# Kernel tuning notes

Hardware: AMD Instinct MI355X
Metric: run time of the kernel (lower is better)

The kernel has to match this reference:

```python
import jax, jax.numpy as jnp
import numpy as np

N = 50000; E = 320000; DIN = 768; D = 256; R = 4; L = 3
B = 64; T = 6; SD = 128; SH = 256; NC = 14; ALPHA = 0.15
NEG = -1e30


def setup_inputs():
    keys = iter(jax.random.split(jax.random.key(0), 64))
    def nrm(shape, s=0.02):
        return s * jax.random.normal(next(keys), shape, dtype=jnp.float32)
    inp = {}
    inp["x"] = jax.random.normal(next(keys), (N, DIN), dtype=jnp.float32)
    inp["edge_index"] = jax.random.randint(next(keys), (2, E), 0, N)
    inp["edge_type"] = jax.random.randint(next(keys), (E,), 0, R)
    inp["batch"] = jnp.sort(jax.random.randint(next(keys), (N,), 0, B))
    inp["sequence"] = jax.random.normal(next(keys), (B, T, SD), dtype=jnp.float32)
    inp["proj_W"] = nrm((D, DIN)); inp["proj_b"] = nrm((D,))
    inp["Wr"] = nrm((L, R, D, D))
    inp["Ws"] = nrm((L, D, D)); inp["bs"] = nrm((L, D))
    inp["att_W1"] = nrm((L, R, D // 2, 2 * D)); inp["att_b1"] = nrm((L, R, D // 2))
    inp["att_W2"] = nrm((L, R, D // 2)); inp["att_b2"] = nrm((L, R))
    inp["emb"] = nrm((L, R, D // 4), 0.1)
    inp["imp"] = jnp.tile(jnp.array([1.2, 1.1, 1.4, 0.9], dtype=jnp.float32), (L, 1))
    inp["ln_g"] = jnp.ones((L, D), jnp.float32); inp["ln_b"] = jnp.zeros((L, D), jnp.float32)
    inp["gm_W1"] = nrm((D // 2, D)); inp["gm_b1"] = nrm((D // 2,))
    inp["gm_W2"] = nrm((D // 4, D // 2)); inp["gm_b2"] = nrm((D // 4,))
    inp["gm_W3"] = nrm((NC, D // 4)); inp["gm_b3"] = nrm((NC,))
    inp["gru_Wih"] = nrm((2, 3 * SH, SD)); inp["gru_Whh"] = nrm((2, 3 * SH, SH))
    inp["gru_bih"] = nrm((2, 3 * SH)); inp["gru_bhh"] = nrm((2, 3 * SH))
    inp["sm_W1"] = nrm((SH, 2 * SH)); inp["sm_b1"] = nrm((SH,))
    inp["sm_W2"] = nrm((SH // 2, SH)); inp["sm_b2"] = nrm((SH // 2,))
    inp["sm_W3"] = nrm((NC, SH // 2)); inp["sm_b3"] = nrm((NC,))
    return inp


def _gru_dir(x, Wih, Whh, bih, bhh):  # x: [B,T,SD] -> [B,T,SH], torch GRU equations
    def step(h, xt):
        gi = xt @ Wih.T + bih
        gh = h @ Whh.T + bhh
        ir, iz, in_ = jnp.split(gi, 3, axis=-1)
        hr, hz, hn = jnp.split(gh, 3, axis=-1)
        r = jax.nn.sigmoid(ir + hr)
        z = jax.nn.sigmoid(iz + hz)
        n = jnp.tanh(in_ + r * hn)
        h = (1.0 - z) * n + z * h
        return h, h
    h0 = jnp.zeros((x.shape[0], Whh.shape[1]), x.dtype)
    _, ys = jax.lax.scan(step, h0, jnp.swapaxes(x, 0, 1))
    return jnp.swapaxes(ys, 0, 1)


def _gnn_layer(h, h0, src, dst, et, Wr, Ws, bs, aW1, ab1, aW2, ab2, emb, imp, g, b):
    ew = jax.nn.softmax(imp)  # layer_edge_importance softmax over R types
    cat = jnp.concatenate([h[dst], h[src]], axis=1)  # [E, 2D] = [x_i, x_j]
    agg = jnp.zeros_like(h)
    for r in range(R):
        tx = h @ Wr[r].T  # [N, D] per-type transform
        s = jax.nn.relu(cat @ aW1[r].T + ab1[r]) @ aW2[r] + ab2[r]  # [E]
        s = jax.nn.leaky_relu(s, 0.2) + jnp.mean(emb[r])
        mask = et == r
        a = jax.nn.softmax(jnp.where(mask, s, NEG))  # softmax over all type-r edges (dim=0 in torch)
        a = jnp.where(mask, a, 0.0)
        msg = jax.ops.segment_sum(a[:, None] * tx[src], dst, num_segments=h.shape[0])
        agg = agg + ew[r] * msg
    out = (1.0 - ALPHA) * agg + h @ Ws.T + bs + ALPHA * h0
    mu = jnp.mean(out, axis=-1, keepdims=True)
    var = jnp.var(out, axis=-1, keepdims=True)
    out = (out - mu) / jnp.sqrt(var + 1e-5) * g + b  # LayerNorm (eps=1e-5)
    return jax.nn.gelu(out, approximate=False)


def _forward(x, sequence, proj_W, proj_b, Wr, Ws, bs, att_W1, att_b1, att_W2, att_b2, emb, imp, ln_g, ln_b, gm_W1, gm_b1, gm_W2, gm_b2, gm_W3, gm_b3, gru_Wih, gru_Whh, gru_bih, gru_bhh, sm_W1, sm_b1, sm_W2, sm_b2, sm_W3, sm_b3, edge_index, edge_type, batch):
    # sequence branch: bidirectional GRU, avg+max pool over time, MLP readout
    fwd = _gru_dir(sequence, gru_Wih[0], gru_Whh[0], gru_bih[0], gru_bhh[0])
    bwd = _gru_dir(sequence[:, ::-1], gru_Wih[1], gru_Whh[1], gru_bih[1], gru_bhh[1])[:, ::-1]
    seq_out = jnp.concatenate([fwd, bwd], axis=-1)  # [B, T, 2*SH]
    z = jnp.mean(seq_out, axis=1) + jnp.max(seq_out, axis=1)
    z = jax.nn.relu(z @ sm_W1.T + sm_b1)
    z = jax.nn.relu(z @ sm_W2.T + sm_b2)
    seq_logits = z @ sm_W3.T + sm_b3
    # graph branch
    src, dst = edge_index[0], edge_index[1]
    h = x @ proj_W.T + proj_b
    h0 = h
    for i in range(L):
        h = _gnn_layer(h, h0, src, dst, edge_type, Wr[i], Ws[i], bs[i], att_W1[i], att_b1[i], att_W2[i], att_b2[i], emb[i], imp[i], ln_g[i], ln_b[i])
    sums = jax.ops.segment_sum(h, batch, num_segments=B)
    cnt = jax.ops.segment_sum(jnp.ones((h.shape[0],), h.dtype), batch, num_segments=B)
    pooled = sums / jnp.clip(cnt, 1.0)[:, None]  # global_mean_pool
    gz = jax.nn.relu(pooled @ gm_W1.T + gm_b1)
    gz = jax.nn.relu(gz @ gm_W2.T + gm_b2)
    graph_logits = gz @ gm_W3.T + gm_b3
    return graph_logits + seq_logits


def reference(x, edge_index, edge_type, batch, sequence, proj_W, proj_b, Wr, Ws, bs, att_W1, att_b1, att_W2, att_b2, emb, imp, ln_g, ln_b, gm_W1, gm_b1, gm_W2, gm_b2, gm_W3, gm_b3, gru_Wih, gru_Whh, gru_bih, gru_bhh, sm_W1, sm_b1, sm_W2, sm_b2, sm_W3, sm_b3):
    return _forward(x, sequence, proj_W, proj_b, Wr, Ws, bs, att_W1, att_b1, att_W2, att_b2, emb, imp, ln_g, ln_b, gm_W1, gm_b1, gm_W2, gm_b2, gm_W3, gm_b3, gru_Wih, gru_Whh, gru_bih, gru_bhh, sm_W1, sm_b1, sm_W2, sm_b2, sm_W3, sm_b3, edge_index, edge_type, batch)
```

## Files before the change

kernel.cpp:

```cpp
#include <hip/hip_runtime.h>
#include <math.h>

#define N_NODES 50000
#define E_EDGES 320000
#define DIN_    768
#define D_      256
#define R_TYPES 4
#define L_LAYERS 3
#define BATCH_  64
#define T_STEPS 6
#define SD_     128
#define SH_     256
#define NC_     14
#define ALPHA_  0.15f
#define NBLK_B  1250
#define POOL_CHUNK 256
#define E_PAD   (E_EDGES + 256)
#define SCAN_BLK 49
#define NCAT    (D_ + R_TYPES * D_)

typedef __bf16 bf16_t;
typedef bf16_t bf16x8_t __attribute__((ext_vector_type(8)));
typedef bf16_t bf16x4_t __attribute__((ext_vector_type(4)));
typedef float  f32x4_t  __attribute__((ext_vector_type(4)));

__device__ __forceinline__ f32x4_t mfma16(bf16x8_t a, bf16x8_t b, f32x4_t c) {
    return __builtin_amdgcn_mfma_f32_16x16x32_bf16(a, b, c, 0, 0, 0);
}

__global__ void f2b_kernel(const float* __restrict__ src, bf16_t* __restrict__ dst, int n4)
{
    for (int i = blockIdx.x * blockDim.x + threadIdx.x; i < n4; i += gridDim.x * blockDim.x) {
        float4 v = ((const float4*)src)[i];
        bf16_t o[4] = {(bf16_t)v.x, (bf16_t)v.y, (bf16_t)v.z, (bf16_t)v.w};
        *(ulong1*)&dst[i * 4] = *(ulong1*)o;
    }
}

__global__ void pack_wcat_kernel(const float* __restrict__ Ws, const float* __restrict__ Wr,
                                 bf16_t* __restrict__ Wcat)
{
    int total = L_LAYERS * NCAT * D_;
    for (int i = blockIdx.x * blockDim.x + threadIdx.x; i < total; i += gridDim.x * blockDim.x) {
        int l = i / (NCAT * D_);
        int rem = i - l * NCAT * D_;
        int row = rem / D_, k = rem - row * D_;
        float v = (row < D_) ? Ws[((size_t)l * D_ + row) * D_ + k]
                             : Wr[((size_t)l * R_TYPES * D_ + (row - D_)) * D_ + k];
        Wcat[i] = (bf16_t)v;
    }
}

__global__ void transpose2_kernel(const float* __restrict__ in, float* __restrict__ out, int R, int C)
{
    int total = 2 * R * C;
    for (int i = blockIdx.x * blockDim.x + threadIdx.x; i < total; i += gridDim.x * blockDim.x) {
        int dir = i / (R * C);
        int rem = i - dir * R * C;
        int r = rem / C, c = rem - r * C;
        out[dir * R * C + c * R + r] = in[i];
    }
}

__global__ __launch_bounds__(256) void proj_mfma(
    const float* __restrict__ A, const bf16_t* __restrict__ W,
    const float* __restrict__ bias, float* __restrict__ outf,
    bf16_t* __restrict__ outb, int M)
{
    __shared__ bf16_t As[64][44];
    __shared__ bf16_t Bs[256][44];
    const int m0 = blockIdx.x * 64;
    const int tid = threadIdx.x;
    const int wave = tid >> 6, lane = tid & 63;
    const int q = lane >> 4, c = lane & 15;
    const int srow = tid >> 2, skq = tid & 3;

    f32x4_t acc[4][4] = {};
    for (int k0 = 0; k0 < DIN_; k0 += 32) {
        {
            int m = m0 + srow;
            bf16_t tmp[8] = {};
            if (m < M) {
                float4 v0 = *(const float4*)&A[(size_t)m * DIN_ + k0 + skq * 8];
                float4 v1 = *(const float4*)&A[(size_t)m * DIN_ + k0 + skq * 8 + 4];
                tmp[0] = (bf16_t)v0.x; tmp[1] = (bf16_t)v0.y; tmp[2] = (bf16_t)v0.z; tmp[3] = (bf16_t)v0.w;
                tmp[4] = (bf16_t)v1.x; tmp[5] = (bf16_t)v1.y; tmp[6] = (bf16_t)v1.z; tmp[7] = (bf16_t)v1.w;
            }
            *(bf16x8_t*)&As[srow][skq * 8] = *(bf16x8_t*)tmp;
            #pragma unroll
            for (int i = 0; i < 4; i++) {
                int nrow = srow + 64 * i;
                *(bf16x8_t*)&Bs[nrow][skq * 8] = *(const bf16x8_t*)&W[(size_t)nrow * DIN_ + k0 + skq * 8];
            }
        }
        __syncthreads();
        bf16x8_t af[4], bfv[4];
        #pragma unroll
        for (int mt = 0; mt < 4; mt++) af[mt] = *(const bf16x8_t*)&As[mt * 16 + c][q * 8];
        #pragma unroll
        for (int nt = 0; nt < 4; nt++) bfv[nt] = *(const bf16x8_t*)&Bs[wave * 64 + nt * 16 + c][q * 8];
        #pragma unroll
        for (int mt = 0; mt < 4; mt++)
            #pragma unroll
            for (int nt = 0; nt < 4; nt++)
                acc[mt][nt] = mfma16(af[mt], bfv[nt], acc[mt][nt]);
        __syncthreads();
    }
    #pragma unroll
    for (int nt = 0; nt < 4; nt++) {
        int n = wave * 64 + nt * 16 + c;
        float bv = bias[n];
        #pragma unroll
        for (int mt = 0; mt < 4; mt++) {
            #pragma unroll
            for (int j = 0; j < 4; j++) {
                int m = m0 + mt * 16 + q * 4 + j;
                if (m < M) {
                    float v = acc[mt][nt][j] + bv;
                    outf[(size_t)m * D_ + n] = v;
                    outb[(size_t)m * D_ + n] = (bf16_t)v;
                }
            }
        }
    }
}

__global__ __launch_bounds__(256) void linear_dual_mfma(
    const bf16_t* __restrict__ A, const bf16_t* __restrict__ W,
    const float* __restrict__ bias, float* __restrict__ outf,
    bf16_t* __restrict__ outb, int M)
{
    __shared__ bf16_t As[64][44];
    __shared__ bf16_t Bs[64][44];
    const int m0 = blockIdx.x * 64;
    const int n0 = blockIdx.y * 64;
    const int tid = threadIdx.x;
    const int wave = tid >> 6, lane = tid & 63;
    const int wy = wave >> 1, wx = wave & 1;
    const int q = lane >> 4, c = lane & 15;
    const int srow = tid >> 2, skq = tid & 3;

    f32x4_t acc[2][2] = {};
    for (int k0 = 0; k0 < D_; k0 += 32) {
        {
            int m = m0 + srow;
            bf16x8_t av = {};
            if (m < M) av = *(const bf16x8_t*)&A[(size_t)m * D_ + k0 + skq * 8];
            *(bf16x8_t*)&As[srow][skq * 8] = av;
            *(bf16x8_t*)&Bs[srow][skq * 8] = *(const bf16x8_t*)&W[(size_t)(n0 + srow) * D_ + k0 + skq * 8];
        }
        __syncthreads();
        bf16x8_t af[2], bfv[2];
        #pragma unroll
        for (int mt = 0; mt < 2; mt++) af[mt] = *(const bf16x8_t*)&As[wy * 32 + mt * 16 + c][q * 8];
        #pragma unroll
        for (int nt = 0; nt < 2; nt++) bfv[nt] = *(const bf16x8_t*)&Bs[wx * 32 + nt * 16 + c][q * 8];
        #pragma unroll
        for (int mt = 0; mt < 2; mt++)
            #pragma unroll
            for (int nt = 0; nt < 2; nt++)
                acc[mt][nt] = mfma16(af[mt], bfv[nt], acc[mt][nt]);
        __syncthreads();
    }
    #pragma unroll
    for (int mt = 0; mt < 2; mt++) {
        #pragma unroll
        for (int nt = 0; nt < 2; nt++) {
            int n = n0 + wx * 32 + nt * 16 + c;
            float bv = (n < D_) ? bias[n] : 0.0f;
            #pragma unroll
            for (int j = 0; j < 4; j++) {
                int m = m0 + wy * 32 + mt * 16 + q * 4 + j;
                if (m < M) {
                    float v = acc[mt][nt][j] + bv;
                    if (n < D_) outf[(size_t)m * D_ + n] = v;
                    else        outb[(size_t)m * (R_TYPES * D_) + (n - D_)] = (bf16_t)v;
                }
            }
        }
    }
}

__global__ __launch_bounds__(256) void bucket_count2(const int* __restrict__ et,
                                                     int* __restrict__ blockCnt)
{
    int b = blockIdx.x, tid = threadIdx.x;
    int r = et[b * 256 + tid];
    int lane = tid & 63, wv = tid >> 6;
    __shared__ int wcnt[4][4];
    #pragma unroll
    for (int t = 0; t < 4; t++) {
        unsigned long long m = __ballot(r == t);
        if (lane == 0) wcnt[wv][t] = __popcll(m);
    }
    __syncthreads();
    if (tid < 4)
        blockCnt[b * 4 + tid] = wcnt[0][tid] + wcnt[1][tid] + wcnt[2][tid] + wcnt[3][tid];
}

__global__ void bucket_scan(const int* __restrict__ blockCnt, int* __restrict__ boffP,
                            int* __restrict__ cnt, int* __restrict__ basePerBlock,
                            int* __restrict__ bsrc, int* __restrict__ bdst)
{
    __shared__ int tot[4];
    int t = threadIdx.x;
    if (t < 4) {
        int s = 0;
        for (int b = 0; b < NBLK_B; b++) s += blockCnt[b * 4 + t];
        tot[t] = s;
    }
    __syncthreads();
    if (t == 0) {
        int o = 0;
        for (int r = 0; r < 4; r++) {
            boffP[r] = o; cnt[r] = tot[r];
            o += (tot[r] + 63) & ~63;
        }
        boffP[4] = o;
    }
    __syncthreads();
    if (t < 4) {
        int run = boffP[t];
        for (int b = 0; b < NBLK_B; b++) { basePerBlock[b * 4 + t] = run; run += blockCnt[b * 4 + t]; }
    }
    __syncthreads();
    for (int r = 0; r < 4; r++) {
        int s = boffP[r] + cnt[r], e = boffP[r + 1];
        for (int i = s + t; i < e; i += 64) { bsrc[i] = 0; bdst[i] = 0; }
    }
}

__global__ __launch_bounds__(256) void bucket_scatter2(
    const int* __restrict__ ei, const int* __restrict__ et,
    const int* __restrict__ basePerBlock, int* __restrict__ bsrc, int* __restrict__ bdst)
{
    int b = blockIdx.x, tid = threadIdx.x;
    int e = b * 256 + tid;
    int r = et[e];
    int lane = tid & 63, wv = tid >> 6;
    __shared__ int wcnt[4][4];
    int myrank = 0;
    unsigned long long ltmask = (1ull << lane) - 1ull;
    #pragma unroll
    for (int t = 0; t < 4; t++) {
        unsigned long long m = __ballot(r == t);
        if (r == t) myrank = __popcll(m & ltmask);
        if (lane == 0) wcnt[wv][t] = __popcll(m);
    }
    __syncthreads();
    int wbase = 0;
    for (int w = 0; w < wv; w++) wbase += wcnt[w][r];
    int pos = basePerBlock[b * 4 + r] + wbase + myrank;
    bsrc[pos] = ei[e];
    bdst[pos] = ei[E_EDGES + e];
}

__global__ void embmean_kernel(const float* __restrict__ emb, float* __restrict__ em)
{
    int lr = threadIdx.x;
    if (lr < L_LAYERS * R_TYPES) {
        float s = 0.0f;
        for (int k = 0; k < 64; k++) s += emb[lr * 64 + k];
        em[lr] = s / 64.0f;
    }
}

__global__ __launch_bounds__(256) void deg_count_kernel(
    const int* __restrict__ bdst, const int* __restrict__ boffP, const int* __restrict__ cnt,
    int* __restrict__ deg)
{
    __shared__ int sb[5], sc[4];
    if (threadIdx.x < 5) sb[threadIdx.x] = boffP[threadIdx.x];
    if (threadIdx.x < 4) sc[threadIdx.x] = cnt[threadIdx.x];
    __syncthreads();
    int total = sb[4];
    for (int p = blockIdx.x * blockDim.x + threadIdx.x; p < total; p += gridDim.x * blockDim.x) {
        int r = 0; while (r < 3 && p >= sb[r + 1]) r++;
        if (p - sb[r] < sc[r]) atomicAdd(&deg[bdst[p]], 1);
    }
}

__global__ __launch_bounds__(256) void scan1_kernel(const int* __restrict__ deg,
                                                    int* __restrict__ rowptr, int* __restrict__ blockSum)
{
    __shared__ int sdata[256];
    int b = blockIdx.x, t = threadIdx.x;
    int idx0 = b * 1024 + t * 4;
    int d[4];
    #pragma unroll
    for (int j = 0; j < 4; j++) d[j] = (idx0 + j < N_NODES) ? deg[idx0 + j] : 0;
    int tsum = d[0] + d[1] + d[2] + d[3];
    sdata[t] = tsum;
    __syncthreads();
    for (int off = 1; off < 256; off <<= 1) {
        int v = (t >= off) ? sdata[t - off] : 0;
        __syncthreads();
        sdata[t] += v;
        __syncthreads();
    }
    int ex = sdata[t] - tsum;
    int acc = ex;
    #pragma unroll
    for (int j = 0; j < 4; j++) {
        if (idx0 + j < N_NODES) rowptr[idx0 + j] = acc;
        acc += d[j];
    }
    if (t == 255) blockSum[b] = sdata[255];
}

__global__ void scan2_kernel(const int* __restrict__ blockSum, int* __restrict__ blockOff)
{
    if (threadIdx.x == 0) {
        int o = 0;
        for (int b = 0; b < SCAN_BLK; b++) { blockOff[b] = o; o += blockSum[b]; }
    }
}

__global__ __launch_bounds__(256) void scan3_kernel(int* __restrict__ rowptr,
                                                    const int* __restrict__ blockOff,
                                                    int* __restrict__ cursor)
{
    int idx = blockIdx.x * blockDim.x + threadIdx.x;
    if (idx < N_NODES) {
        int v = rowptr[idx] + blockOff[idx >> 10];
        rowptr[idx] = v; cursor[idx] = v;
    }
    if (idx == 0) rowptr[N_NODES] = E_EDGES;
}

__global__ __launch_bounds__(256) void csr_scatter_kernel(
    const int* __restrict__ bsrc, const int* __restrict__ bdst,
    const int* __restrict__ boffP, const int* __restrict__ cnt,
    int* __restrict__ cursor, int* __restrict__ csrSrc, int* __restrict__ csrPos)
{
    __shared__ int sb[5], sc[4];
    if (threadIdx.x < 5) sb[threadIdx.x] = boffP[threadIdx.x];
    if (threadIdx.x < 4) sc[threadIdx.x] = cnt[threadIdx.x];
    __syncthreads();
    int total = sb[4];
    for (int p = blockIdx.x * blockDim.x + threadIdx.x; p < total; p += gridDim.x * blockDim.x) {
        int r = 0; while (r < 3 && p >= sb[r + 1]) r++;
        if (p - sb[r] < sc[r]) {
            int pos = atomicAdd(&cursor[bdst[p]], 1);
            csrSrc[pos] = bsrc[p];
            csrPos[pos] = p;
        }
    }
}

__global__ __launch_bounds__(256) void attn_mfma(
    const bf16_t* __restrict__ hb, const int* __restrict__ bsrc, const int* __restrict__ bdst,
    const int* __restrict__ boffP, const int* __restrict__ cnt, int l,
    const bf16_t* __restrict__ W1base, const float* __restrict__ b1base,
    const float* __restrict__ W2base, const float* __restrict__ b2base,
    const float* __restrict__ em, float* __restrict__ sbuf)
{
    const int p0 = blockIdx.x * 64;
    if (p0 >= boffP[4]) return;
    int r = 0;
    while (r < 3 && p0 >= boffP[r + 1]) r++;
    const int lr = l * R_TYPES + r;
    const int base = boffP[r];
    const int cnt_r = cnt[r];
    const bf16_t* W1 = W1base + (size_t)lr * 128 * 512;
    const float*  b1 = b1base + lr * 128;
    const float*  W2 = W2base + lr * 128;

    __shared__ int nd_d[64], nd_s[64];
    __shared__ bf16_t Acat[64][44];
    __shared__ bf16_t Bs[128][44];
    const int tid = threadIdx.x;
    if (tid < 64) nd_d[tid] = bdst[p0 + tid];
    else if (tid < 128) nd_s[tid - 64] = bsrc[p0 + tid - 64];
    __syncthreads();
    const int wave = tid >> 6, lane = tid & 63;
    const int q = lane >> 4, c = lane & 15;
    const int srow = tid >> 2, skq = tid & 3;

    f32x4_t acc[8] = {};
    for (int ks = 0; ks < 16; ks++) {
        {
            int node = (ks < 8) ? nd_d[srow] : nd_s[srow];
            int koffm = (ks & 7) * 32 + skq * 8;
            *(bf16x8_t*)&Acat[srow][skq * 8] = *(const bf16x8_t*)&hb[(size_t)node * D_ + koffm];
            #pragma unroll
            for (int s = 0; s < 2; s++) {
                int slot = tid + s * 256;
                int nrow = slot >> 2, nkq = slot & 3;
                *(bf16x8_t*)&Bs[nrow][nkq * 8] = *(const bf16x8_t*)&W1[(size_t)nrow * 512 + ks * 32 + nkq * 8];
            }
        }
        __syncthreads();
        bf16x8_t af = *(const bf16x8_t*)&Acat[wave * 16 + c][q * 8];
        #pragma unroll
        for (int nt = 0; nt < 8; nt++) {
            bf16x8_t bfv = *(const bf16x8_t*)&Bs[nt * 16 + c][q * 8];
            acc[nt] = mfma16(af, bfv, acc[nt]);
        }
        __syncthreads();
    }
    float part[4] = {0, 0, 0, 0};
    #pragma unroll
    for (int nt = 0; nt < 8; nt++) {
        int n = nt * 16 + c;
        float b1v = b1[n], w2v = W2[n];
        #pragma unroll
        for (int j = 0; j < 4; j++) {
            float v = acc[nt][j] + b1v;
            v = v > 0.0f ? v : 0.0f;
            part[j] += v * w2v;
        }
    }
    #pragma unroll
    for (int j = 0; j < 4; j++) {
        #pragma unroll
        for (int mask = 1; mask <= 8; mask <<= 1)
            part[j] += __shfl_xor(part[j], mask);
    }
    if (c == 0) {
        float b2v = b2base[lr], emv = em[lr];
        #pragma unroll
        for (int j = 0; j < 4; j++) {
            int p = p0 + wave * 16 + q * 4 + j;
            bool valid = (p - base) < cnt_r;
            float sv = part[j] + b2v;
            sv = sv > 0.0f ? sv : 0.2f * sv;
            sbuf[p] = valid ? (sv + emv) : -1e30f;
        }
    }
}

__device__ __forceinline__ unsigned fkey(float f) {
    unsigned u = __float_as_uint(f);
    return (u & 0x80000000u) ? ~u : (u | 0x80000000u);
}
__device__ __forceinline__ float fkey_inv(unsigned k) {
    unsigned u = (k & 0x80000000u) ? (k ^ 0x80000000u) : ~k;
    return __uint_as_float(u);
}

__global__ void bucket_max_kernel(const float* __restrict__ sbuf, const int* __restrict__ boffP,
                                  unsigned* __restrict__ redl)
{
    int r = blockIdx.y;
    int lo = boffP[r], hi = boffP[r + 1];
    float m = -1e30f;
    for (int i = lo + blockIdx.x * blockDim.x + threadIdx.x; i < hi; i += gridDim.x * blockDim.x)
        m = fmaxf(m, sbuf[i]);
    for (int o = 32; o; o >>= 1) m = fmaxf(m, __shfl_down(m, o));
    __shared__ float wm[4];
    int lane = threadIdx.x & 63, wv = threadIdx.x >> 6;
    if (lane == 0) wm[wv] = m;
    __syncthreads();
    if (threadIdx.x == 0) {
        float b = fmaxf(fmaxf(wm[0], wm[1]), fmaxf(wm[2], wm[3]));
        atomicMax(&redl[r * 2], fkey(b));
    }
}

__global__ void bucket_sum_kernel(const float* __restrict__ sbuf, const int* __restrict__ boffP,
                                  unsigned* __restrict__ redl)
{
    int r = blockIdx.y;
    int lo = boffP[r], hi = boffP[r + 1];
    float mxf = fkey_inv(redl[r * 2]);
    float s = 0.0f;
    for (int i = lo + blockIdx.x * blockDim.x + threadIdx.x; i < hi; i += gridDim.x * blockDim.x)
        s += expf(sbuf[i] - mxf);
    for (int o = 32; o; o >>= 1) s += __shfl_down(s, o);
    __shared__ float wm[4];
    int lane = threadIdx.x & 63, wv = threadIdx.x >> 6;
    if (lane == 0) wm[wv] = s;
    __syncthreads();
    if (threadIdx.x == 0) atomicAdd((float*)&redl[r * 2 + 1], wm[0] + wm[1] + wm[2] + wm[3]);
}

__global__ __launch_bounds__(256) void msg_ln_gelu_kernel(
    const float* __restrict__ sbuf, const bf16_t* __restrict__ txAll,
    const int* __restrict__ csrSrc, const int* __restrict__ csrPos,
    const int* __restrict__ rowptr, const int* __restrict__ boffP,
    const unsigned* __restrict__ redl, const float* __restrict__ imp, int l,
    const float* __restrict__ accb, const float* __restrict__ h0,
    const float* __restrict__ g, const float* __restrict__ bvec,
    float* __restrict__ h, bf16_t* __restrict__ hb)
{
    __shared__ float smx[4], sinv[4], scoef[4];
    __shared__ int sb[5];
    if (threadIdx.x == 0) {
        float e0 = expf(imp[l * 4 + 0]), e1 = expf(imp[l * 4 + 1]);
        float e2 = expf(imp[l * 4 + 2]), e3 = expf(imp[l * 4 + 3]);
        float den = e0 + e1 + e2 + e3;
        float ews[4] = {e0 / den, e1 / den, e2 / den, e3 / den};
        for (int r = 0; r < 4; r++) {
            smx[r] = fkey_inv(redl[r * 2]);
            sinv[r] = 1.0f / ((const float*)redl)[r * 2 + 1];
            scoef[r] = (1.0f - ALPHA_) * ews[r];
        }
        for (int r = 0; r <= 4; r++) sb[r] = boffP[r];
    }
    __syncthreads();
    int n = blockIdx.x * 4 + (threadIdx.x >> 6);
    if (n >= N_NODES) return;
    int lane = threadIdx.x & 63;
    int c4 = lane * 4;
    float msg[4] = {0, 0, 0, 0};
    int i0 = rowptr[n], i1 = rowptr[n + 1];
    for (int i = i0; i < i1; i++) {
        int src = csrSrc[i];
        int p = csrPos[i];
        int r = 0; while (r < 3 && p >= sb[r + 1]) r++;
        float a = expf(sbuf[p] - smx[r]) * sinv[r] * scoef[r];
        bf16x4_t tv = *(const bf16x4_t*)&txAll[(size_t)src * (R_TYPES * D_) + r * D_ + c4];
        msg[0] += a * (float)tv[0];
        msg[1] += a * (float)tv[1];
        msg[2] += a * (float)tv[2];
        msg[3] += a * (float)tv[3];
    }
    float4 ac = *(const float4*)&accb[(size_t)n * D_ + c4];
    float4 hz = *(const float4*)&h0[(size_t)n * D_ + c4];
    float v[4];
    v[0] = msg[0] + ac.x + ALPHA_ * hz.x;
    v[1] = msg[1] + ac.y + ALPHA_ * hz.y;
    v[2] = msg[2] + ac.z + ALPHA_ * hz.z;
    v[3] = msg[3] + ac.w + ALPHA_ * hz.w;
    float sum = v[0] + v[1] + v[2] + v[3];
    #pragma unroll
    for (int o = 32; o; o >>= 1) sum += __shfl_down(sum, o);
    sum = __shfl(sum, 0);
    float mean = sum * (1.0f / 256.0f);
    float sq = 0.0f;
    #pragma unroll
    for (int j = 0; j < 4; j++) { float d = v[j] - mean; sq += d * d; }
    #pragma unroll
    for (int o = 32; o; o >>= 1) sq += __shfl_down(sq, o);
    sq = __shfl(sq, 0);
    float rstd = rsqrtf(sq * (1.0f / 256.0f) + 1e-5f);
    float4 gg = *(const float4*)&g[c4];
    float4 bb = *(const float4*)&bvec[c4];
    float ga[4] = {gg.x, gg.y, gg.z, gg.w};
    float ba[4] = {bb.x, bb.y, bb.z, bb.w};
    float outv[4];
    bf16_t outb[4];
    #pragma unroll
    for (int j = 0; j < 4; j++) {
        float x = (v[j] - mean) * rstd * ga[j] + ba[j];
        float ge = 0.5f * x * (1.0f + erff(x * 0.7071067811865475f));
        outv[j] = ge;
        outb[j] = (bf16_t)ge;
    }
    *(float4*)&h[(size_t)n * D_ + c4] = *(float4*)outv;
    *(bf16x4_t*)&hb[(size_t)n * D_ + c4] = *(bf16x4_t*)outb;
}

__global__ __launch_bounds__(256) void pool_seg_kernel(
    const float* __restrict__ h, const int* __restrict__ batch,
    float* __restrict__ pooled, float* __restrict__ cntb, int Nn)
{
    int start = blockIdx.x * POOL_CHUNK;
    if (start >= Nn) return;
    int end = start + POOL_CHUNK; if (end > Nn) end = Nn;
    int c = threadIdx.x;
    __shared__ int bseg[POOL_CHUNK];
    if (start + c < Nn) bseg[c] = batch[start + c];
    __syncthreads();
    float acc = 0.0f;
    int cur = bseg[0];
    int segcnt = 0;
    for (int node = start; node < end; node++) {
        int b = bseg[node - start];
        if (b != cur) {
            atomicAdd(&pooled[cur * D_ + c], acc);
            if (c == 0) atomicAdd(&cntb[cur], (float)segcnt);
            acc = 0.0f; segcnt = 0; cur = b;
        }
        acc += h[(size_t)node * D_ + c];
        segcnt++;
    }
    atomicAdd(&pooled[cur * D_ + c], acc);
    if (c == 0) atomicAdd(&cntb[cur], (float)segcnt);
}

__global__ __launch_bounds__(256) void final_mlp_kernel(
    const float* __restrict__ pooled, const float* __restrict__ cntb,
    const float* __restrict__ W1, const float* __restrict__ b1,
    const float* __restrict__ W2, const float* __restrict__ b2,
    const float* __restrict__ W3, const float* __restrict__ b3,
    const float* __restrict__ seqlg, float* __restrict__ out)
{
    int b = blockIdx.x;
    int t = threadIdx.x;
    __shared__ float p[256];
    __shared__ float z1[128];
    __shared__ float z2[64];
    float c = cntb[b]; c = c < 1.0f ? 1.0f : c;
    p[t] = pooled[b * 256 + t] / c;
    __syncthreads();
    if (t < 128) {
        float s = b1[t];
        for (int k = 0; k < 256; k++) s += p[k] * W1[t * 256 + k];
        z1[t] = s > 0.0f ? s : 0.0f;
    }
    __syncthreads();
    if (t < 64) {
        float s = b2[t];
        for (int k = 0; k < 128; k++) s += z1[k] * W2[t * 128 + k];
        z2[t] = s > 0.0f ? s : 0.0f;
    }
    __syncthreads();
    if (t < NC_) {
        float s = b3[t];
        for (int k = 0; k < 64; k++) s += z2[k] * W3[t * 64 + k];
        out[b * NC_ + t] = s + seqlg[b * NC_ + t];
    }
}

__global__ __launch_bounds__(768) void gru_gi_kernel(
    const float* __restrict__ seq, const float* __restrict__ WihT,
    const float* __restrict__ bih, float* __restrict__ gi)
{
    int blk = blockIdx.x;
    int dir = blk >> 6, b = blk & 63;
    __shared__ float xt[T_STEPS * SD_];
    int j = threadIdx.x;
    xt[j] = seq[(size_t)b * T_STEPS * SD_ + j];
    __syncthreads();
    const float* Wt = WihT + (size_t)dir * SD_ * 768;
    float av[T_STEPS] = {};
    for (int k = 0; k < SD_; k++) {
        float w = Wt[(size_t)k * 768 + j];
        #pragma unroll
        for (int t = 0; t < T_STEPS; t++) av[t] += xt[t * SD_ + k] * w;
    }
    float bv = bih[dir * 768 + j];
    for (int t = 0; t < T_STEPS; t++)
        gi[(((size_t)blk) * T_STEPS + t) * 768 + j] = av[t] + bv;
}

__global__ __launch_bounds__(768) void gru_step2(
    const float* __restrict__ gi, const float* __restrict__ WhhT,
    const float* __restrict__ bhh, float* __restrict__ hstate,
    float* __restrict__ outs, int t)
{
    int blk = blockIdx.x;
    int dir = blk >> 6;
    int tin = dir ? (T_STEPS - 1 - t) : t;
    __shared__ float hs[SH_];
    __shared__ float gh[768];
    int j = threadIdx.x;
    if (j < SH_) hs[j] = hstate[(size_t)blk * SH_ + j];
    __syncthreads();
    const float* Wt = WhhT + (size_t)dir * SH_ * 768;
    float a = bhh[dir * 768 + j];
    for (int k = 0; k < SH_; k++)
        a += hs[k] * Wt[(size_t)k * 768 + j];
    gh[j] = a;
    __syncthreads();
    if (j < SH_) {
        size_t gib = (((size_t)blk) * T_STEPS + tin) * 768;
        float r = 1.0f / (1.0f + expf(-(gi[gib + j] + gh[j])));
        float z = 1.0f / (1.0f + expf(-(gi[gib + 256 + j] + gh[256 + j])));
        float n = tanhf(gi[gib + 512 + j] + r * gh[512 + j]);
        float hn = (1.0f - z) * n + z * hs[j];
        hstate[(size_t)blk * SH_ + j] = hn;
        outs[(((size_t)blk) * T_STEPS + tin) * SH_ + j] = hn;
    }
}

__global__ __launch_bounds__(256) void seq_mlp_kernel(
    const float* __restrict__ outs, const float* __restrict__ W1, const float* __restrict__ b1,
    const float* __restrict__ W2, const float* __restrict__ b2,
    const float* __restrict__ W3, const float* __restrict__ b3,
    float* __restrict__ seqlg)
{
    int b = blockIdx.x;
    int t = threadIdx.x;
    __shared__ float z[512];
    __shared__ float z1[256];
    __shared__ float z2[128];
    for (int c = t; c < 512; c += 256) {
        int dir = c >> 8, cc = c & 255;
        float mean = 0.0f, mx = -1e30f;
        for (int tt = 0; tt < T_STEPS; tt++) {
            float v = outs[(((size_t)dir * 64 + b) * T_STEPS + tt) * SH_ + cc];
            mean += v; mx = fmaxf(mx, v);
        }
        z[c] = mean * (1.0f / T_STEPS) + mx;
    }
    __syncthreads();
    {
        float s = b1[t];
        for (int k = 0; k < 512; k++) s += z[k] * W1[t * 512 + k];
        z1[t] = s > 0.0f ? s : 0.0f;
    }
    __syncthreads();
    if (t < 128) {
        float s = b2[t];
        for (int k = 0; k < 256; k++) s += z1[k] * W2[t * 256 + k];
        z2[t] = s > 0.0f ? s : 0.0f;
    }
    __syncthreads();
    if (t < NC_) {
        float s = b3[t];
        for (int k = 0; k < 128; k++) s += z2[k] * W3[t * 128 + k];
        seqlg[b * NC_ + t] = s;
    }
}

extern "C" void kernel_launch(void* const* d_in, const int* in_sizes, int n_in,
                              void* d_out, int out_size, void* d_ws, size_t ws_size,
                              hipStream_t stream)
{
    const float* x      = (const float*)d_in[0];
    const int*   ei     = (const int*)d_in[1];
    const int*   et     = (const int*)d_in[2];
    const int*   batch  = (const int*)d_in[3];
    const float* seq    = (const float*)d_in[4];
    const float* proj_W = (const float*)d_in[5];
    const float* proj_b = (const float*)d_in[6];
    const float* Wr     = (const float*)d_in[7];
    const float* Ws     = (const float*)d_in[8];
    const float* bs     = (const float*)d_in[9];
    const float* aW1    = (const float*)d_in[10];
    const float* ab1    = (const float*)d_in[11];
    const float* aW2    = (const float*)d_in[12];
    const float* ab2    = (const float*)d_in[13];
    const float* emb    = (const float*)d_in[14];
    const float* imp    = (const float*)d_in[15];
    const float* ln_g   = (const float*)d_in[16];
    const float* ln_b   = (const float*)d_in[17];
    const float* gmW1   = (const float*)d_in[18];
    const float* gmb1   = (const float*)d_in[19];
    const float* gmW2   = (const float*)d_in[20];
    const float* gmb2   = (const float*)d_in[21];
    const float* gmW3   = (const float*)d_in[22];
    const float* gmb3   = (const float*)d_in[23];
    const float* gWih   = (const float*)d_in[24];
    const float* gWhh   = (const float*)d_in[25];
    const float* gbih   = (const float*)d_in[26];
    const float* gbhh   = (const float*)d_in[27];
    const float* smW1   = (const float*)d_in[28];
    const float* smb1   = (const float*)d_in[29];
    const float* smW2   = (const float*)d_in[30];
    const float* smb2   = (const float*)d_in[31];
    const float* smW3   = (const float*)d_in[32];
    const float* smb3   = (const float*)d_in[33];
    float* out = (float*)d_out;

    char* ws = (char*)d_ws;
    size_t o = 0;
    auto alloc = [&](size_t bytes) -> void* {
        void* p = ws + o;
        o += (bytes + 1023) & ~(size_t)1023;
        return p;
    };
    float*  h0     = (float*)alloc(sizeof(float) * (size_t)N_NODES * D_);
    float*  h      = (float*)alloc(sizeof(float) * (size_t)N_NODES * D_);
    float*  accb   = (float*)alloc(sizeof(float) * (size_t)N_NODES * D_);
    bf16_t* hbb    = (bf16_t*)alloc(sizeof(bf16_t) * (size_t)N_NODES * D_);
    bf16_t* txAll  = (bf16_t*)alloc(sizeof(bf16_t) * (size_t)N_NODES * R_TYPES * D_);
    bf16_t* projWb = (bf16_t*)alloc(sizeof(bf16_t) * D_ * DIN_);
    bf16_t* Wcat   = (bf16_t*)alloc(sizeof(bf16_t) * L_LAYERS * NCAT * D_);
    bf16_t* aW1b   = (bf16_t*)alloc(sizeof(bf16_t) * L_LAYERS * R_TYPES * 128 * 512);
    float*  sbuf   = (float*)alloc(sizeof(float) * E_PAD);
    int*    bsrc   = (int*)alloc(sizeof(int) * E_PAD);
    int*    bdst   = (int*)alloc(sizeof(int) * E_PAD);
    int*    boffP  = (int*)alloc(sizeof(int) * 8);
    int*    cnt    = (int*)alloc(sizeof(int) * 8);
    int*    blockCnt = (int*)alloc(sizeof(int) * NBLK_B * 4);
    int*    basePerBlock = (int*)alloc(sizeof(int) * NBLK_B * 4);
    int*    deg    = (int*)alloc(sizeof(int) * N_NODES);
    int*    rowptr = (int*)alloc(sizeof(int) * (N_NODES + 8));
    int*    cursor = (int*)alloc(sizeof(int) * N_NODES);
    int*    blockSum = (int*)alloc(sizeof(int) * 64);
    int*    blockOff = (int*)alloc(sizeof(int) * 64);
    int*    csrSrc = (int*)alloc(sizeof(int) * E_EDGES);
    int*    csrPos = (int*)alloc(sizeof(int) * E_EDGES);
    unsigned* red  = (unsigned*)alloc(sizeof(unsigned) * 32);
    float*  em     = (float*)alloc(sizeof(float) * 16);
    float*  seqlg  = (float*)alloc(sizeof(float) * BATCH_ * NC_);
    float*  WihT   = (float*)alloc(sizeof(float) * 2 * SD_ * 768);
    float*  WhhT   = (float*)alloc(sizeof(float) * 2 * SH_ * 768);
    float*  gi     = (float*)alloc(sizeof(float) * 2 * BATCH_ * T_STEPS * 768);
    float*  gruH   = (float*)alloc(sizeof(float) * 2 * BATCH_ * SH_);
    float*  gruO   = (float*)alloc(sizeof(float) * 2 * BATCH_ * T_STEPS * SH_);
    float*  pooled = (float*)alloc(sizeof(float) * BATCH_ * D_);
    float*  cntb   = (float*)alloc(sizeof(float) * BATCH_);
    (void)ws_size; (void)in_sizes; (void)n_in; (void)out_size;

    hipMemsetAsync(red, 0, 32 * sizeof(unsigned), stream);
    hipMemsetAsync(gruH, 0, 2 * BATCH_ * SH_ * sizeof(float), stream);
    hipMemsetAsync(pooled, 0, BATCH_ * D_ * sizeof(float), stream);
    hipMemsetAsync(cntb, 0, BATCH_ * sizeof(float), stream);
    hipMemsetAsync(deg, 0, N_NODES * sizeof(int), stream);

    f2b_kernel<<<64, 256, 0, stream>>>(proj_W, projWb, D_ * DIN_ / 4);
    pack_wcat_kernel<<<512, 256, 0, stream>>>(Ws, Wr, Wcat);
    f2b_kernel<<<256, 256, 0, stream>>>(aW1, aW1b, L_LAYERS * R_TYPES * 128 * 512 / 4);
    transpose2_kernel<<<96, 256, 0, stream>>>(gWih, WihT, 768, SD_);
    transpose2_kernel<<<192, 256, 0, stream>>>(gWhh, WhhT, 768, SH_);

    bucket_count2<<<NBLK_B, 256, 0, stream>>>(et, blockCnt);
    bucket_scan<<<1, 64, 0, stream>>>(blockCnt, boffP, cnt, basePerBlock, bsrc, bdst);
    bucket_scatter2<<<NBLK_B, 256, 0, stream>>>(ei, et, basePerBlock, bsrc, bdst);
    embmean_kernel<<<1, 64, 0, stream>>>(emb, em);

    deg_count_kernel<<<1024, 256, 0, stream>>>(bdst, boffP, cnt, deg);
    scan1_kernel<<<SCAN_BLK, 256, 0, stream>>>(deg, rowptr, blockSum);
    scan2_kernel<<<1, 64, 0, stream>>>(blockSum, blockOff);
    scan3_kernel<<<(N_NODES + 255) / 256, 256, 0, stream>>>(rowptr, blockOff, cursor);
    csr_scatter_kernel<<<1024, 256, 0, stream>>>(bsrc, bdst, boffP, cnt, cursor, csrSrc, csrPos);

    gru_gi_kernel<<<128, 768, 0, stream>>>(seq, WihT, gbih, gi);
    for (int t = 0; t < T_STEPS; t++)
        gru_step2<<<128, 768, 0, stream>>>(gi, WhhT, gbhh, gruH, gruO, t);
    seq_mlp_kernel<<<BATCH_, 256, 0, stream>>>(gruO, smW1, smb1, smW2, smb2, smW3, smb3, seqlg);

    const int MB = (N_NODES + 63) / 64;
    proj_mfma<<<MB, 256, 0, stream>>>(x, projWb, proj_b, h0, hbb, N_NODES);
    const int ATTN_BLKS = E_PAD / 64;
    for (int l = 0; l < L_LAYERS; l++) {
        linear_dual_mfma<<<dim3(MB, NCAT / 64), 256, 0, stream>>>(
            hbb, Wcat + (size_t)l * NCAT * D_, bs + l * D_, accb, txAll, N_NODES);
        attn_mfma<<<ATTN_BLKS, 256, 0, stream>>>(hbb, bsrc, bdst, boffP, cnt, l,
                                                 aW1b, ab1, aW2, ab2, em, sbuf);
        bucket_max_kernel<<<dim3(256, 4), 256, 0, stream>>>(sbuf, boffP, red + l * 8);
        bucket_sum_kernel<<<dim3(256, 4), 256, 0, stream>>>(sbuf, boffP, red + l * 8);
        msg_ln_gelu_kernel<<<(N_NODES + 3) / 4, 256, 0, stream>>>(
            sbuf, txAll, csrSrc, csrPos, rowptr, boffP, red + l * 8, imp, l,
            accb, h0, ln_g + l * D_, ln_b + l * D_, h, hbb);
    }

    pool_seg_kernel<<<(N_NODES + POOL_CHUNK - 1) / POOL_CHUNK, 256, 0, stream>>>(h, batch, pooled, cntb, N_NODES);
    final_mlp_kernel<<<BATCH_, 256, 0, stream>>>(pooled, cntb, gmW1, gmb1, gmW2, gmb2, gmW3, gmb3, seqlg, out);
}
```

Baseline: 1.663 ms.

## Fuse GRU steps, pre-convert x to bf16, drop fp32 layer output

Merges the GRU input projection and all time steps into a single kernel that keeps the hidden state in shared memory, removing per-step launches. The input x is converted to bf16 once and the projection GEMM is split into a 2D grid of 64x64 tiles. The fp32 copy of the layer output is no longer written, and mean pooling reads the bf16 copy instead. This adds an extra conversion pass over x and slightly lowers pooling precision.

```diff
diff --git a/kernel.cpp b/kernel.cpp
--- a/kernel.cpp
+++ b/kernel.cpp
@@ -62,59 +62,52 @@
     }
 }
 
-__global__ __launch_bounds__(256) void proj_mfma(
-    const float* __restrict__ A, const bf16_t* __restrict__ W,
+__global__ __launch_bounds__(256) void proj_mfma3(
+    const bf16_t* __restrict__ A, const bf16_t* __restrict__ W,
     const float* __restrict__ bias, float* __restrict__ outf,
     bf16_t* __restrict__ outb, int M)
 {
     __shared__ bf16_t As[64][44];
-    __shared__ bf16_t Bs[256][44];
+    __shared__ bf16_t Bs[64][44];
     const int m0 = blockIdx.x * 64;
+    const int n0 = blockIdx.y * 64;
     const int tid = threadIdx.x;
     const int wave = tid >> 6, lane = tid & 63;
+    const int wy = wave >> 1, wx = wave & 1;
     const int q = lane >> 4, c = lane & 15;
     const int srow = tid >> 2, skq = tid & 3;
 
-    f32x4_t acc[4][4] = {};
+    f32x4_t acc[2][2] = {};
     for (int k0 = 0; k0 < DIN_; k0 += 32) {
         {
             int m = m0 + srow;
-            bf16_t tmp[8] = {};
-            if (m < M) {
-                float4 v0 = *(const float4*)&A[(size_t)m * DIN_ + k0 + skq * 8];
-                float4 v1 = *(const float4*)&A[(size_t)m * DIN_ + k0 + skq * 8 + 4];
-                tmp[0] = (bf16_t)v0.x; tmp[1] = (bf16_t)v0.y; tmp[2] = (bf16_t)v0.z; tmp[3] = (bf16_t)v0.w;
-                tmp[4] = (bf16_t)v1.x; tmp[5] = (bf16_t)v1.y; tmp[6] = (bf16_t)v1.z; tmp[7] = (bf16_t)v1.w;
-            }
-            *(bf16x8_t*)&As[srow][skq * 8] = *(bf16x8_t*)tmp;
+            bf16x8_t av = {};
+            if (m < M) av = *(const bf16x8_t*)&A[(size_t)m * DIN_ + k0 + skq * 8];
+            *(bf16x8_t*)&As[srow][skq * 8] = av;
+            *(bf16x8_t*)&Bs[srow][skq * 8] = *(const bf16x8_t*)&W[(size_t)(n0 + srow) * DIN_ + k0 + skq * 8];
+        }
+        __syncthreads();
+        bf16x8_t af[2], bfv[2];
+        #pragma unroll
+        for (int mt = 0; mt < 2; mt++) af[mt] = *(const bf16x8_t*)&As[wy * 32 + mt * 16 + c][q * 8];
+        #pragma unroll
+        for (int nt = 0; nt < 2; nt++) bfv[nt] = *(const bf16x8_t*)&Bs[wx * 32 + nt * 16 + c][q * 8];
+        #pragma unroll
+        for (int mt = 0; mt < 2; mt++)
             #pragma unroll
-            for (int i = 0; i < 4; i++) {
-                int nrow = srow + 64 * i;
-                *(bf16x8_t*)&Bs[nrow][skq * 8] = *(const bf16x8_t*)&W[(size_t)nrow * DIN_ + k0 + skq * 8];
-            }
-        }
-        __syncthreads();
-        bf16x8_t af[4], bfv[4];
-        #pragma unroll
-        for (int mt = 0; mt < 4; mt++) af[mt] = *(const bf16x8_t*)&As[mt * 16 + c][q * 8];
-        #pragma unroll
-        for (int nt = 0; nt < 4; nt++) bfv[nt] = *(const bf16x8_t*)&Bs[wave * 64 + nt * 16 + c][q * 8];
-        #pragma unroll
-        for (int mt = 0; mt < 4; mt++)
-            #pragma unroll
-            for (int nt = 0; nt < 4; nt++)
+            for (int nt = 0; nt < 2; nt++)
                 acc[mt][nt] = mfma16(af[mt], bfv[nt], acc[mt][nt]);
         __syncthreads();
     }
     #pragma unroll
-    for (int nt = 0; nt < 4; nt++) {
-        int n = wave * 64 + nt * 16 + c;
-        float bv = bias[n];
-        #pragma unroll
-        for (int mt = 0; mt < 4; mt++) {
+    for (int mt = 0; mt < 2; mt++) {
+        #pragma unroll
+        for (int nt = 0; nt < 2; nt++) {
+            int n = n0 + wx * 32 + nt * 16 + c;
+            float bv = bias[n];
             #pragma unroll
             for (int j = 0; j < 4; j++) {
-                int m = m0 + mt * 16 + q * 4 + j;
+                int m = m0 + wy * 32 + mt * 16 + q * 4 + j;
                 if (m < M) {
                     float v = acc[mt][nt][j] + bv;
                     outf[(size_t)m * D_ + n] = v;
@@ -482,7 +475,7 @@
     const unsigned* __restrict__ redl, const float* __restrict__ imp, int l,
     const float* __restrict__ accb, const float* __restrict__ h0,
     const float* __restrict__ g, const float* __restrict__ bvec,
-    float* __restrict__ h, bf16_t* __restrict__ hb)
+    bf16_t* __restrict__ hb)
 {
     __shared__ float smx[4], sinv[4], scoef[4];
     __shared__ int sb[5];
@@ -539,21 +532,18 @@
     float4 bb = *(const float4*)&bvec[c4];
     float ga[4] = {gg.x, gg.y, gg.z, gg.w};
     float ba[4] = {bb.x, bb.y, bb.z, bb.w};
-    float outv[4];
     bf16_t outb[4];
     #pragma unroll
     for (int j = 0; j < 4; j++) {
         float x = (v[j] - mean) * rstd * ga[j] + ba[j];
         float ge = 0.5f * x * (1.0f + erff(x * 0.7071067811865475f));
-        outv[j] = ge;
         outb[j] = (bf16_t)ge;
     }
-    *(float4*)&h[(size_t)n * D_ + c4] = *(float4*)outv;
     *(bf16x4_t*)&hb[(size_t)n * D_ + c4] = *(bf16x4_t*)outb;
 }
 
 __global__ __launch_bounds__(256) void pool_seg_kernel(
-    const float* __restrict__ h, const int* __restrict__ batch,
+    const bf16_t* __restrict__ hb, const int* __restrict__ batch,
     float* __restrict__ pooled, float* __restrict__ cntb, int Nn)
 {
     int start = blockIdx.x * POOL_CHUNK;
@@ -573,7 +563,7 @@
             if (c == 0) atomicAdd(&cntb[cur], (float)segcnt);
             acc = 0.0f; segcnt = 0; cur = b;
         }
-        acc += h[(size_t)node * D_ + c];
+        acc += (float)hb[(size_t)node * D_ + c];
         segcnt++;
     }
     atomicAdd(&pooled[cur * D_ + c], acc);
@@ -614,55 +604,48 @@
     }
 }
 
-__global__ __launch_bounds__(768) void gru_gi_kernel(
+__global__ __launch_bounds__(768) void gru_full(
     const float* __restrict__ seq, const float* __restrict__ WihT,
-    const float* __restrict__ bih, float* __restrict__ gi)
+    const float* __restrict__ bih, const float* __restrict__ WhhT,
+    const float* __restrict__ bhh, float* __restrict__ outs)
 {
     int blk = blockIdx.x;
     int dir = blk >> 6, b = blk & 63;
     __shared__ float xt[T_STEPS * SD_];
+    __shared__ float hs[SH_];
+    __shared__ float gh[768];
+    __shared__ float gg[768];
     int j = threadIdx.x;
     xt[j] = seq[(size_t)b * T_STEPS * SD_ + j];
-    __syncthreads();
-    const float* Wt = WihT + (size_t)dir * SD_ * 768;
+    if (j < SH_) hs[j] = 0.0f;
+    __syncthreads();
+    const float* Wti = WihT + (size_t)dir * SD_ * 768;
     float av[T_STEPS] = {};
     for (int k = 0; k < SD_; k++) {
-        float w = Wt[(size_t)k * 768 + j];
+        float w = Wti[(size_t)k * 768 + j];
         #pragma unroll
         for (int t = 0; t < T_STEPS; t++) av[t] += xt[t * SD_ + k] * w;
     }
-    float bv = bih[dir * 768 + j];
-    for (int t = 0; t < T_STEPS; t++)
-        gi[(((size_t)blk) * T_STEPS + t) * 768 + j] = av[t] + bv;
-}
-
-__global__ __launch_bounds__(768) void gru_step2(
-    const float* __restrict__ gi, const float* __restrict__ WhhT,
-    const float* __restrict__ bhh, float* __restrict__ hstate,
-    float* __restrict__ outs, int t)
-{
-    int blk = blockIdx.x;
-    int dir = blk >> 6;
-    int tin = dir ? (T_STEPS - 1 - t) : t;
-    __shared__ float hs[SH_];
-    __shared__ float gh[768];
-    int j = threadIdx.x;
-    if (j < SH_) hs[j] = hstate[(size_t)blk * SH_ + j];
-    __syncthreads();
-    const float* Wt = WhhT + (size_t)dir * SH_ * 768;
-    float a = bhh[dir * 768 + j];
-    for (int k = 0; k < SH_; k++)
-        a += hs[k] * Wt[(size_t)k * 768 + j];
-    gh[j] = a;
-    __syncthreads();
-    if (j < SH_) {
-        size_t gib = (((size_t)blk) * T_STEPS + tin) * 768;
-        float r = 1.0f / (1.0f + expf(-(gi[gib + j] + gh[j])));
-        float z = 1.0f / (1.0f + expf(-(gi[gib + 256 + j] + gh[256 + j])));
-        float n = tanhf(gi[gib + 512 + j] + r * gh[512 + j]);
-        float hn = (1.0f - z) * n + z * hs[j];
-        hstate[(size_t)blk * SH_ + j] = hn;
-        outs[(((size_t)blk) * T_STEPS + tin) * SH_ + j] = hn;
+    float bihv = bih[dir * 768 + j];
+    float bhhv = bhh[dir * 768 + j];
+    const float* Wth = WhhT + (size_t)dir * SH_ * 768;
+    for (int t = 0; t < T_STEPS; t++) {
+        int tin = dir ? (T_STEPS - 1 - t) : t;
+        float a = bhhv;
+        for (int k = 0; k < SH_; k++)
+            a += hs[k] * Wth[(size_t)k * 768 + j];
+        gh[j] = a;
+        gg[j] = av[tin] + bihv;
+        __syncthreads();
+        if (j < SH_) {
+            float r = 1.0f / (1.0f + expf(-(gg[j] + gh[j])));
+            float z = 1.0f / (1.0f + expf(-(gg[256 + j] + gh[256 + j])));
+            float n = tanhf(gg[512 + j] + r * gh[512 + j]);
+            float hn = (1.0f - z) * n + z * hs[j];
+            hs[j] = hn;
+            outs[(((size_t)blk) * T_STEPS + tin) * SH_ + j] = hn;
+        }
+        __syncthreads();
     }
 }
 
@@ -754,9 +737,9 @@
         return p;
     };
     float*  h0     = (float*)alloc(sizeof(float) * (size_t)N_NODES * D_);
-    float*  h      = (float*)alloc(sizeof(float) * (size_t)N_NODES * D_);
     float*  accb   = (float*)alloc(sizeof(float) * (size_t)N_NODES * D_);
     bf16_t* hbb    = (bf16_t*)alloc(sizeof(bf16_t) * (size_t)N_NODES * D_);
+    bf16_t* xb     = (bf16_t*)alloc(sizeof(bf16_t) * (size_t)N_NODES * DIN_);
     bf16_t* txAll  = (bf16_t*)alloc(sizeof(bf16_t) * (size_t)N_NODES * R_TYPES * D_);
     bf16_t* projWb = (bf16_t*)alloc(sizeof(bf16_t) * D_ * DIN_);
     bf16_t* Wcat   = (bf16_t*)alloc(sizeof(bf16_t) * L_LAYERS * NCAT * D_);
@@ -780,19 +763,17 @@
     float*  seqlg  = (float*)alloc(sizeof(float) * BATCH_ * NC_);
     float*  WihT   = (float*)alloc(sizeof(float) * 2 * SD_ * 768);
     float*  WhhT   = (float*)alloc(sizeof(float) * 2 * SH_ * 768);
-    float*  gi     = (float*)alloc(sizeof(float) * 2 * BATCH_ * T_STEPS * 768);
-    float*  gruH   = (float*)alloc(sizeof(float) * 2 * BATCH_ * SH_);
     float*  gruO   = (float*)alloc(sizeof(float) * 2 * BATCH_ * T_STEPS * SH_);
     float*  pooled = (float*)alloc(sizeof(float) * BATCH_ * D_);
     float*  cntb   = (float*)alloc(sizeof(float) * BATCH_);
     (void)ws_size; (void)in_sizes; (void)n_in; (void)out_size;
 
     hipMemsetAsync(red, 0, 32 * sizeof(unsigned), stream);
-    hipMemsetAsync(gruH, 0, 2 * BATCH_ * SH_ * sizeof(float), stream);
     hipMemsetAsync(pooled, 0, BATCH_ * D_ * sizeof(float), stream);
     hipMemsetAsync(cntb, 0, BATCH_ * sizeof(float), stream);
     hipMemsetAsync(deg, 0, N_NODES * sizeof(int), stream);
 
+    f2b_kernel<<<2048, 256, 0, stream>>>(x, xb, N_NODES * DIN_ / 4);
     f2b_kernel<<<64, 256, 0, stream>>>(proj_W, projWb, D_ * DIN_ / 4);
     pack_wcat_kernel<<<512, 256, 0, stream>>>(Ws, Wr, Wcat);
     f2b_kernel<<<256, 256, 0, stream>>>(aW1, aW1b, L_LAYERS * R_TYPES * 128 * 512 / 4);
@@ -810,13 +791,11 @@
     scan3_kernel<<<(N_NODES + 255) / 256, 256, 0, stream>>>(rowptr, blockOff, cursor);
     csr_scatter_kernel<<<1024, 256, 0, stream>>>(bsrc, bdst, boffP, cnt, cursor, csrSrc, csrPos);
 
-    gru_gi_kernel<<<128, 768, 0, stream>>>(seq, WihT, gbih, gi);
-    for (int t = 0; t < T_STEPS; t++)
-        gru_step2<<<128, 768, 0, stream>>>(gi, WhhT, gbhh, gruH, gruO, t);
+    gru_full<<<128, 768, 0, stream>>>(seq, WihT, gbih, WhhT, gbhh, gruO);
     seq_mlp_kernel<<<BATCH_, 256, 0, stream>>>(gruO, smW1, smb1, smW2, smb2, smW3, smb3, seqlg);
 
     const int MB = (N_NODES + 63) / 64;
-    proj_mfma<<<MB, 256, 0, stream>>>(x, projWb, proj_b, h0, hbb, N_NODES);
+    proj_mfma3<<<dim3(MB, D_ / 64), 256, 0, stream>>>(xb, projWb, proj_b, h0, hbb, N_NODES);
     const int ATTN_BLKS = E_PAD / 64;
     for (int l = 0; l < L_LAYERS; l++) {
         linear_dual_mfma<<<dim3(MB, NCAT / 64), 256, 0, stream>>>(
@@ -827,9 +806,9 @@
         bucket_sum_kernel<<<dim3(256, 4), 256, 0, stream>>>(sbuf, boffP, red + l * 8);
         msg_ln_gelu_kernel<<<(N_NODES + 3) / 4, 256, 0, stream>>>(
             sbuf, txAll, csrSrc, csrPos, rowptr, boffP, red + l * 8, imp, l,
-            accb, h0, ln_g + l * D_, ln_b + l * D_, h, hbb);
-    }
-
-    pool_seg_kernel<<<(N_NODES + POOL_CHUNK - 1) / POOL_CHUNK, 256, 0, stream>>>(h, batch, pooled, cntb, N_NODES);
+            accb, h0, ln_g + l * D_, ln_b + l * D_, hbb);
+    }
+
+    pool_seg_kernel<<<(N_NODES + POOL_CHUNK - 1) / POOL_CHUNK, 256, 0, stream>>>(hbb, batch, pooled, cntb, N_NODES);
     final_mlp_kernel<<<BATCH_, 256, 0, stream>>>(pooled, cntb, gmW1, gmb1, gmW2, gmb2, gmW3, gmb3, seqlg, out);
 }
```

Result: faster. 1.572 ms (-5.5%).
